# Kernel optimization log

Measured on AMD Instinct MI355X. Metric: run time of the kernel, lower is better.

## Reference

```python
import jax, jax.numpy as jnp
import numpy as np
import math

D_MODEL = 512
NHEAD = 8
D_HEAD = D_MODEL // NHEAD
D_FF = 2048
N_LAYERS = 6
B, S = 8, 2048
EPS = 1e-5


def _layernorm(x, g, b):
    mu = jnp.mean(x, axis=-1, keepdims=True)
    var = jnp.mean(jnp.square(x - mu), axis=-1, keepdims=True)
    return (x - mu) * jax.lax.rsqrt(var + EPS) * g + b


def setup_inputs() -> dict:
    key = jax.random.key(0)
    ks = jax.random.split(key, 10)
    sc = 1.0 / math.sqrt(D_MODEL)
    scf = 1.0 / math.sqrt(D_FF)
    return {
        "x": jax.random.normal(ks[0], (B, S, D_MODEL), jnp.float32),
        "wq": jax.random.normal(ks[1], (N_LAYERS, D_MODEL, D_MODEL), jnp.float32) * sc,
        "wk": jax.random.normal(ks[2], (N_LAYERS, D_MODEL, D_MODEL), jnp.float32) * sc,
        "wv": jax.random.normal(ks[3], (N_LAYERS, D_MODEL, D_MODEL), jnp.float32) * sc,
        "wo": jax.random.normal(ks[4], (N_LAYERS, D_MODEL, D_MODEL), jnp.float32) * sc,
        "w1": jax.random.normal(ks[5], (N_LAYERS, D_MODEL, D_FF), jnp.float32) * sc,
        "b1": jnp.zeros((N_LAYERS, D_FF), jnp.float32),
        "w2": jax.random.normal(ks[6], (N_LAYERS, D_FF, D_MODEL), jnp.float32) * scf,
        "b2": jnp.zeros((N_LAYERS, D_MODEL), jnp.float32),
        "g1": jnp.ones((N_LAYERS, D_MODEL), jnp.float32),
        "beta1": jnp.zeros((N_LAYERS, D_MODEL), jnp.float32),
        "g2": jnp.ones((N_LAYERS, D_MODEL), jnp.float32),
        "beta2": jnp.zeros((N_LAYERS, D_MODEL), jnp.float32),
    }


def reference(x, wq, wk, wv, wo, w1, b1, w2, b2, g1, beta1, g2, beta2):
    scale = 1.0 / math.sqrt(D_HEAD)
    for i in range(N_LAYERS):
        # NOTE: faithful to torch .view(B, nhead, -1, d_head) WITHOUT transpose
        q = (x @ wq[i]).reshape(B, NHEAD, S, D_HEAD)
        k = (x @ wk[i]).reshape(B, NHEAD, S, D_HEAD)
        v = (x @ wv[i]).reshape(B, NHEAD, S, D_HEAD)
        u = jnp.einsum("bhsd,bhtd->bhst", q, k) * scale
        attn = jax.nn.softmax(u, axis=-1)
        o = jnp.einsum("bhst,bhtd->bhsd", attn, v).reshape(B, S, D_MODEL)
        x = _layernorm(x + o @ wo[i], g1[i], beta1[i])
        f = jax.nn.relu(x @ w1[i] + b1[i]) @ w2[i] + b2[i]
        x = _layernorm(x + f, g2[i], beta2[i])
    return x
```

## Files before the change

### kernel.cpp

```cpp
#include <hip/hip_runtime.h>
#include <hip/hip_bf16.h>
#include <stdint.h>

typedef __bf16 bf16_t;
typedef bf16_t bf16x8 __attribute__((ext_vector_type(8)));
typedef bf16_t bf16x4 __attribute__((ext_vector_type(4)));
typedef float  f32x4  __attribute__((ext_vector_type(4)));

#define AS1 __attribute__((address_space(1)))
#define AS3 __attribute__((address_space(3)))

__device__ __forceinline__ void gload_lds16(const void* g, void* l) {
  __builtin_amdgcn_global_load_lds((const AS1 void*)g, (AS3 void*)l, 16, 0, 0);
}

__device__ __forceinline__ float fast_exp2(float x) {
#if __has_builtin(__builtin_amdgcn_exp2f)
  return __builtin_amdgcn_exp2f(x);
#else
  return exp2f(x);
#endif
}

#define QSCALE 0.1803368801111204f

template <int RELU, int BIAS, int QKV>
__global__ __launch_bounds__(256) void gemm_bt(const bf16_t* __restrict__ A,
                                               const bf16_t* __restrict__ Bt,
                                               const float* __restrict__ bias,
                                               bf16_t* __restrict__ Cv,
                                               int M, int N, int K, int ldc) {
  __shared__ __align__(16) char smem[65536];
  const int t = threadIdx.x;
  const int l = t & 63;
  const int w = t >> 6;
  const int wm = w >> 1, wn = w & 1;
  const int lr = l & 15, lg = l >> 4;
  const long m0 = (long)blockIdx.y * 128;
  const long n0 = (long)blockIdx.x * 128;

  const bf16_t* asrc[4];
  const bf16_t* bsrc[4];
#pragma unroll
  for (int it = 0; it < 4; ++it) {
    int y = it * 4096 + t * 16;
    int row = y >> 7;
    int col = ((y & 127) ^ ((row & 7) << 4)) >> 1;
    asrc[it] = A + (m0 + row) * (long)K + col;
    bsrc[it] = Bt + (n0 + row) * (long)K + col;
  }

  auto stage = [&](int buf) {
    char* sb = smem + buf * 32768;
#pragma unroll
    for (int it = 0; it < 4; ++it) {
      gload_lds16(asrc[it], sb + it * 4096 + t * 16);
      gload_lds16(bsrc[it], sb + 16384 + it * 4096 + t * 16);
      asrc[it] += 64;
      bsrc[it] += 64;
    }
  };

  f32x4 acc[4][4] = {};

  stage(0);
  __syncthreads();
  const int nt = K >> 6;
  int buf = 0;
  for (int kt = 0; kt < nt; ++kt) {
    if (kt + 1 < nt) stage(buf ^ 1);
    char* sb = smem + buf * 32768;
#pragma unroll
    for (int kk = 0; kk < 2; ++kk) {
      const int c2 = (kk * 32 + lg * 8) * 2;
      bf16x8 a[4], b[4];
#pragma unroll
      for (int i = 0; i < 4; ++i) {
        int ra = wm * 64 + i * 16 + lr;
        a[i] = *(const bf16x8*)(sb + ((ra * 128 + c2) ^ ((ra & 7) << 4)));
        int rb = wn * 64 + i * 16 + lr;
        b[i] = *(const bf16x8*)(sb + 16384 + ((rb * 128 + c2) ^ ((rb & 7) << 4)));
      }
      __builtin_amdgcn_s_setprio(1);
#pragma unroll
      for (int i = 0; i < 4; ++i)
#pragma unroll
        for (int j = 0; j < 4; ++j)
          acc[i][j] = __builtin_amdgcn_mfma_f32_16x16x32_bf16(a[i], b[j], acc[i][j], 0, 0, 0);
      __builtin_amdgcn_s_setprio(0);
    }
    __syncthreads();
    buf ^= 1;
  }

  float bv[4];
  if (BIAS) {
#pragma unroll
    for (int j = 0; j < 4; ++j) bv[j] = bias[n0 + wn * 64 + j * 16 + lr];
  }
#pragma unroll
  for (int i = 0; i < 4; ++i) {
    long rowb = m0 + wm * 64 + i * 16 + lg * 4;
#pragma unroll
    for (int j = 0; j < 4; ++j) {
      int colbase = (int)n0 + wn * 64 + j * 16;
      bf16_t* outp;
      int coll;
      if (QKV) {
        outp = Cv + (size_t)(colbase >> 9) * 8388608;
        coll = (colbase & 511) + lr;
      } else {
        outp = Cv;
        coll = colbase + lr;
      }
#pragma unroll
      for (int r = 0; r < 4; ++r) {
        float v = acc[i][j][r];
        if (BIAS) v += bv[j];
        if (RELU) v = v > 0.f ? v : 0.f;
        outp[(rowb + r) * (long)ldc + coll] = (bf16_t)v;
      }
    }
  }
}

__global__ __launch_bounds__(256) void attn_fa(const bf16_t* __restrict__ qg,
                                               const bf16_t* __restrict__ kg,
                                               const bf16_t* __restrict__ vg,
                                               bf16_t* __restrict__ og) {
  __shared__ __align__(16) char smem[32768];
  const int t = threadIdx.x, l = t & 63, w = t >> 6;
  const int lr = l & 15, lg = l >> 4;
  const long hoff = (long)blockIdx.x * 131072;
  const int q0 = blockIdx.y * 128 + w * 32;
  const uint32_t LDSB = (uint32_t)(uintptr_t)(AS3 char*)smem;

  bf16x8 qf[2][2];
#pragma unroll
  for (int nf = 0; nf < 2; ++nf)
#pragma unroll
    for (int kk = 0; kk < 2; ++kk)
      qf[nf][kk] = *(const bf16x8*)(qg + hoff + (long)(q0 + nf * 16 + lr) * 64 + kk * 32 + lg * 8);

  const bf16_t* ksrc[2];
#pragma unroll
  for (int i = 0; i < 2; ++i) {
    int y = i * 4096 + t * 16;
    int row = y >> 7;
    int col = ((y & 127) ^ ((row & 7) << 4)) >> 1;
    ksrc[i] = kg + hoff + (long)row * 64 + col;
  }
  const bf16_t* vsrc[2];
#pragma unroll
  for (int i = 0; i < 2; ++i) {
    int y = i * 4096 + t * 16;
    int kk = y >> 12;
    int nj = (y >> 10) & 3;
    int jhi = (y >> 9) & 1;
    int lgs = (y >> 7) & 3;
    int r = (y >> 5) & 3;
    int ch = (y >> 4) & 1;
    int kv = kk * 32 + jhi * 16 + lgs * 4 + r;
    int d0 = nj * 16 + ch * 8;
    vsrc[i] = vg + hoff + (long)kv * 64 + d0;
  }

  auto stage = [&](int buf) {
    char* sb = smem + buf * 16384;
    gload_lds16(ksrc[0], sb + t * 16);
    gload_lds16(ksrc[1], sb + 4096 + t * 16);
    gload_lds16(vsrc[0], sb + 8192 + t * 16);
    gload_lds16(vsrc[1], sb + 12288 + t * 16);
    ksrc[0] += 4096; ksrc[1] += 4096; vsrc[0] += 4096; vsrc[1] += 4096;
  };

  f32x4 oacc[2][4] = {};
  f32x4 lacc[2] = {};
  bf16x8 onesf;
#pragma unroll
  for (int j = 0; j < 8; ++j) onesf[j] = (bf16_t)1.0f;

  stage(0);
  __syncthreads();
  int buf = 0;
  for (int ti = 0; ti < 32; ++ti) {
    if (ti < 31) stage(buf ^ 1);
    char* sb = smem + buf * 16384;

    f32x4 sT[4][2] = {};
#pragma unroll
    for (int kk = 0; kk < 2; ++kk) {
      const int c2 = (kk * 32 + lg * 8) * 2;
      bf16x8 kf[4];
#pragma unroll
      for (int mf = 0; mf < 4; ++mf) {
        int rk = mf * 16 + lr;
        kf[mf] = *(const bf16x8*)(sb + ((rk * 128 + c2) ^ ((rk & 7) << 4)));
      }
      __builtin_amdgcn_s_setprio(1);
#pragma unroll
      for (int mf = 0; mf < 4; ++mf)
#pragma unroll
        for (int nf = 0; nf < 2; ++nf)
          sT[mf][nf] = __builtin_amdgcn_mfma_f32_16x16x32_bf16(kf[mf], qf[nf][kk], sT[mf][nf], 0, 0, 0);
      __builtin_amdgcn_s_setprio(0);
    }

    bf16x8 pa[2][2];
#pragma unroll
    for (int m2 = 0; m2 < 2; ++m2)
#pragma unroll
      for (int kk = 0; kk < 2; ++kk)
#pragma unroll
        for (int jh = 0; jh < 2; ++jh)
#pragma unroll
          for (int r = 0; r < 4; ++r)
            pa[m2][kk][jh * 4 + r] = (bf16_t)fast_exp2(sT[2 * kk + jh][m2][r]);

#pragma unroll
    for (int kk = 0; kk < 2; ++kk) {
      uint32_t va = LDSB + (uint32_t)buf * 16384u + 8192u + (uint32_t)kk * 4096u + (uint32_t)l * 8u;
      bf16x4 v00, v01, v10, v11, v20, v21, v30, v31;
      asm volatile(
          "ds_read_b64_tr_b16 %0, %8 offset:0\n\t"
          "ds_read_b64_tr_b16 %1, %8 offset:512\n\t"
          "ds_read_b64_tr_b16 %2, %8 offset:1024\n\t"
          "ds_read_b64_tr_b16 %3, %8 offset:1536\n\t"
          "ds_read_b64_tr_b16 %4, %8 offset:2048\n\t"
          "ds_read_b64_tr_b16 %5, %8 offset:2560\n\t"
          "ds_read_b64_tr_b16 %6, %8 offset:3072\n\t"
          "ds_read_b64_tr_b16 %7, %8 offset:3584\n\t"
          "s_waitcnt lgkmcnt(0)"
          : "=&v"(v00), "=&v"(v01), "=&v"(v10), "=&v"(v11),
            "=&v"(v20), "=&v"(v21), "=&v"(v30), "=&v"(v31)
          : "v"(va));
      __builtin_amdgcn_sched_barrier(0);
      bf16x8 vf[4];
      vf[0] = __builtin_shufflevector(v00, v01, 0, 1, 2, 3, 4, 5, 6, 7);
      vf[1] = __builtin_shufflevector(v10, v11, 0, 1, 2, 3, 4, 5, 6, 7);
      vf[2] = __builtin_shufflevector(v20, v21, 0, 1, 2, 3, 4, 5, 6, 7);
      vf[3] = __builtin_shufflevector(v30, v31, 0, 1, 2, 3, 4, 5, 6, 7);
      __builtin_amdgcn_s_setprio(1);
#pragma unroll
      for (int m2 = 0; m2 < 2; ++m2) {
#pragma unroll
        for (int nj = 0; nj < 4; ++nj)
          oacc[m2][nj] = __builtin_amdgcn_mfma_f32_16x16x32_bf16(pa[m2][kk], vf[nj], oacc[m2][nj], 0, 0, 0);
        lacc[m2] = __builtin_amdgcn_mfma_f32_16x16x32_bf16(pa[m2][kk], onesf, lacc[m2], 0, 0, 0);
      }
      __builtin_amdgcn_s_setprio(0);
    }
    __syncthreads();
    buf ^= 1;
  }

#pragma unroll
  for (int m2 = 0; m2 < 2; ++m2)
#pragma unroll
    for (int r = 0; r < 4; ++r) {
      float inv = 1.f / lacc[m2][r];
      long row = q0 + m2 * 16 + lg * 4 + r;
#pragma unroll
      for (int nj = 0; nj < 4; ++nj)
        og[hoff + row * 64 + nj * 16 + lr] = (bf16_t)(oacc[m2][nj][r] * inv);
    }
}

__global__ __launch_bounds__(256) void transpose_w(const float* __restrict__ src,
                                                   bf16_t* __restrict__ dst,
                                                   int K, int N,
                                                   long dstLayerStride, float scale) {
  __shared__ float tile[32][33];
  const int t = threadIdx.x;
  const int tx = t & 31, ty = t >> 5;
  const long ls = (long)blockIdx.z * K * N;
  const long ld = (long)blockIdx.z * dstLayerStride;
  const int n0 = blockIdx.x * 32, k0 = blockIdx.y * 32;
#pragma unroll
  for (int i = 0; i < 4; ++i)
    tile[ty + i * 8][tx] = src[ls + (long)(k0 + ty + i * 8) * N + n0 + tx];
  __syncthreads();
#pragma unroll
  for (int i = 0; i < 4; ++i)
    dst[ld + (long)(n0 + ty + i * 8) * K + k0 + tx] = (bf16_t)(tile[tx][ty + i * 8] * scale);
}

__global__ __launch_bounds__(256) void init_x(const float* __restrict__ x,
                                              float* __restrict__ xm,
                                              bf16_t* __restrict__ xb) {
  long i = ((long)blockIdx.x * 256 + threadIdx.x) * 8;
  f32x4 a = *(const f32x4*)(x + i);
  f32x4 b = *(const f32x4*)(x + i + 4);
  *(f32x4*)(xm + i) = a;
  *(f32x4*)(xm + i + 4) = b;
  bf16x8 o;
#pragma unroll
  for (int j = 0; j < 4; ++j) { o[j] = (bf16_t)a[j]; o[4 + j] = (bf16_t)b[j]; }
  *(bf16x8*)(xb + i) = o;
}

__global__ __launch_bounds__(256) void resid_ln(const bf16_t* __restrict__ delta,
                                                float* __restrict__ xm,
                                                bf16_t* __restrict__ xb,
                                                const float* __restrict__ g,
                                                const float* __restrict__ b) {
  const int t = threadIdx.x, l = t & 63, w = t >> 6;
  const long row = (long)blockIdx.x * 4 + w;
  const long base = row * 512 + l * 8;
  f32x4 a0 = *(const f32x4*)(xm + base);
  f32x4 a1 = *(const f32x4*)(xm + base + 4);
  bf16x8 dv = *(const bf16x8*)(delta + base);
  float s[8];
  float sum = 0.f, sq = 0.f;
#pragma unroll
  for (int j = 0; j < 4; ++j) {
    s[j] = a0[j] + (float)dv[j];
    s[4 + j] = a1[j] + (float)dv[4 + j];
  }
#pragma unroll
  for (int j = 0; j < 8; ++j) { sum += s[j]; sq += s[j] * s[j]; }
#pragma unroll
  for (int m = 1; m <= 32; m <<= 1) {
    sum += __shfl_xor(sum, m, 64);
    sq += __shfl_xor(sq, m, 64);
  }
  float mu = sum * (1.f / 512.f);
  float var = sq * (1.f / 512.f) - mu * mu;
  float rstd = rsqrtf(var + 1e-5f);
  f32x4 g0 = *(const f32x4*)(g + l * 8);
  f32x4 g1v = *(const f32x4*)(g + l * 8 + 4);
  f32x4 b0 = *(const f32x4*)(b + l * 8);
  f32x4 b1v = *(const f32x4*)(b + l * 8 + 4);
  f32x4 y0, y1;
  bf16x8 yb;
#pragma unroll
  for (int j = 0; j < 4; ++j) {
    y0[j] = (s[j] - mu) * rstd * g0[j] + b0[j];
    y1[j] = (s[4 + j] - mu) * rstd * g1v[j] + b1v[j];
    yb[j] = (bf16_t)y0[j];
    yb[4 + j] = (bf16_t)y1[j];
  }
  *(f32x4*)(xm + base) = y0;
  *(f32x4*)(xm + base + 4) = y1;
  *(bf16x8*)(xb + base) = yb;
}

extern "C" void kernel_launch(void* const* d_in, const int* in_sizes, int n_in,
                              void* d_out, int out_size, void* d_ws, size_t ws_size,
                              hipStream_t stream) {
  const float* x = (const float*)d_in[0];
  const float* wq = (const float*)d_in[1];
  const float* wk = (const float*)d_in[2];
  const float* wv = (const float*)d_in[3];
  const float* wo = (const float*)d_in[4];
  const float* w1 = (const float*)d_in[5];
  const float* b1 = (const float*)d_in[6];
  const float* w2 = (const float*)d_in[7];
  const float* b2 = (const float*)d_in[8];
  const float* g1 = (const float*)d_in[9];
  const float* be1 = (const float*)d_in[10];
  const float* g2 = (const float*)d_in[11];
  const float* be2 = (const float*)d_in[12];

  float* xm = (float*)d_out;
  char* ws = (char*)d_ws;

  const int M = 16384, D = 512, DFF = 2048, NL = 6;
  const size_t sz_small = (size_t)NL * D * D * 2;
  const size_t sz_big = (size_t)NL * D * DFF * 2;
  bf16_t* wqkvt = (bf16_t*)(ws);
  bf16_t* wot = (bf16_t*)(ws + 3 * sz_small);
  bf16_t* w1t = (bf16_t*)(ws + 4 * sz_small);
  bf16_t* w2t = (bf16_t*)(ws + 4 * sz_small + sz_big);
  char* actbase = ws + 4 * sz_small + 2 * sz_big;
  bf16_t* xb = (bf16_t*)(actbase);
  char* R = actbase + (size_t)M * D * 2;
  bf16_t* qb = (bf16_t*)(R);
  bf16_t* kb = (bf16_t*)(R + (size_t)M * D * 2);
  bf16_t* vb = (bf16_t*)(R + 2 * (size_t)M * D * 2);
  bf16_t* ob = (bf16_t*)(R + 3 * (size_t)M * D * 2);
  bf16_t* hb = (bf16_t*)(R);
  bf16_t* tmpb = (bf16_t*)(R + 4 * (size_t)M * D * 2);

  const long LQKV = 1536L * 512;
  transpose_w<<<dim3(D / 32, D / 32, NL), 256, 0, stream>>>(wq, wqkvt, D, D, LQKV, QSCALE);
  transpose_w<<<dim3(D / 32, D / 32, NL), 256, 0, stream>>>(wk, wqkvt + 512 * 512, D, D, LQKV, 1.f);
  transpose_w<<<dim3(D / 32, D / 32, NL), 256, 0, stream>>>(wv, wqkvt + 2 * 512 * 512, D, D, LQKV, 1.f);
  transpose_w<<<dim3(D / 32, D / 32, NL), 256, 0, stream>>>(wo, wot, D, D, (long)D * D, 1.f);
  transpose_w<<<dim3(DFF / 32, D / 32, NL), 256, 0, stream>>>(w1, w1t, D, DFF, (long)D * DFF, 1.f);
  transpose_w<<<dim3(D / 32, DFF / 32, NL), 256, 0, stream>>>(w2, w2t, DFF, D, (long)D * DFF, 1.f);
  init_x<<<4096, 256, 0, stream>>>(x, xm, xb);

  for (int L = 0; L < NL; ++L) {
    const bf16_t* wqkvL = wqkvt + (size_t)L * LQKV;
    const bf16_t* woL = wot + (size_t)L * D * D;
    const bf16_t* w1L = w1t + (size_t)L * D * DFF;
    const bf16_t* w2L = w2t + (size_t)L * D * DFF;

    gemm_bt<0, 0, 1><<<dim3(12, 128), 256, 0, stream>>>(xb, wqkvL, nullptr, qb, M, 1536, D, 512);
    attn_fa<<<dim3(64, 16), 256, 0, stream>>>(qb, kb, vb, ob);
    gemm_bt<0, 0, 0><<<dim3(4, 128), 256, 0, stream>>>(ob, woL, nullptr, tmpb, M, D, D, D);
    resid_ln<<<4096, 256, 0, stream>>>(tmpb, xm, xb, g1 + L * D, be1 + L * D);
    gemm_bt<1, 1, 0><<<dim3(16, 128), 256, 0, stream>>>(xb, w1L, b1 + (size_t)L * DFF, hb, M, DFF, D, DFF);
    gemm_bt<0, 1, 0><<<dim3(4, 128), 256, 0, stream>>>(hb, w2L, b2 + L * D, tmpb, M, D, DFF, D);
    resid_ln<<<4096, 256, 0, stream>>>(tmpb, xm, xb, g2 + L * D, be2 + L * D);
  }
}
```

Measured before the change: 1.649 ms.

## Swizzle block order, add single-buffer GEMM variant, batch V transposed reads

```diff
diff --git a/kernel.cpp b/kernel.cpp
--- a/kernel.cpp
+++ b/kernel.cpp
@@ -24,20 +24,25 @@
 
 #define QSCALE 0.1803368801111204f
 
-template <int RELU, int BIAS, int QKV>
+template <int RELU, int BIAS, int QKV, int DBUF>
 __global__ __launch_bounds__(256) void gemm_bt(const bf16_t* __restrict__ A,
                                                const bf16_t* __restrict__ Bt,
                                                const float* __restrict__ bias,
                                                bf16_t* __restrict__ Cv,
                                                int M, int N, int K, int ldc) {
-  __shared__ __align__(16) char smem[65536];
+  __shared__ __align__(16) char smem[DBUF ? 65536 : 32768];
   const int t = threadIdx.x;
   const int l = t & 63;
   const int w = t >> 6;
   const int wm = w >> 1, wn = w & 1;
   const int lr = l & 15, lg = l >> 4;
-  const long m0 = (long)blockIdx.y * 128;
-  const long n0 = (long)blockIdx.x * 128;
+
+  const int gx = gridDim.x;
+  const int nwg = gx * gridDim.y;
+  const int orig = blockIdx.y * gx + blockIdx.x;
+  const int swz = (orig & 7) * (nwg >> 3) + (orig >> 3);
+  const long m0 = (long)(swz / gx) * 128;
+  const long n0 = (long)(swz % gx) * 128;
 
   const bf16_t* asrc[4];
   const bf16_t* bsrc[4];
@@ -62,14 +67,9 @@
   };
 
   f32x4 acc[4][4] = {};
-
-  stage(0);
-  __syncthreads();
   const int nt = K >> 6;
-  int buf = 0;
-  for (int kt = 0; kt < nt; ++kt) {
-    if (kt + 1 < nt) stage(buf ^ 1);
-    char* sb = smem + buf * 32768;
+
+  auto compute = [&](char* sb) {
 #pragma unroll
     for (int kk = 0; kk < 2; ++kk) {
       const int c2 = (kk * 32 + lg * 8) * 2;
@@ -89,8 +89,25 @@
           acc[i][j] = __builtin_amdgcn_mfma_f32_16x16x32_bf16(a[i], b[j], acc[i][j], 0, 0, 0);
       __builtin_amdgcn_s_setprio(0);
     }
+  };
+
+  if (DBUF) {
+    stage(0);
     __syncthreads();
-    buf ^= 1;
+    int buf = 0;
+    for (int kt = 0; kt < nt; ++kt) {
+      if (kt + 1 < nt) stage(buf ^ 1);
+      compute(smem + buf * 32768);
+      __syncthreads();
+      buf ^= 1;
+    }
+  } else {
+    for (int kt = 0; kt < nt; ++kt) {
+      __syncthreads();
+      stage(0);
+      __syncthreads();
+      compute(smem);
+    }
   }
 
   float bv[4];
@@ -131,8 +148,10 @@
   __shared__ __align__(16) char smem[32768];
   const int t = threadIdx.x, l = t & 63, w = t >> 6;
   const int lr = l & 15, lg = l >> 4;
-  const long hoff = (long)blockIdx.x * 131072;
-  const int q0 = blockIdx.y * 128 + w * 32;
+  const int lin = blockIdx.x;
+  const int swz = (lin & 7) * 128 + (lin >> 3);
+  const long hoff = (long)(swz >> 4) * 131072;
+  const int q0 = (swz & 15) * 128 + w * 32;
   const uint32_t LDSB = (uint32_t)(uintptr_t)(AS3 char*)smem;
 
   bf16x8 qf[2][2];
@@ -206,50 +225,73 @@
       __builtin_amdgcn_s_setprio(0);
     }
 
+    uint32_t va = LDSB + (uint32_t)buf * 16384u + 8192u + (uint32_t)l * 8u;
+    bf16x4 tv0, tv1, tv2, tv3, tv4, tv5, tv6, tv7;
+    bf16x4 tv8, tv9, tva, tvb, tvc, tvd, tve, tvf;
+    asm volatile(
+        "ds_read_b64_tr_b16 %0, %16 offset:0\n\t"
+        "ds_read_b64_tr_b16 %1, %16 offset:512\n\t"
+        "ds_read_b64_tr_b16 %2, %16 offset:1024\n\t"
+        "ds_read_b64_tr_b16 %3, %16 offset:1536\n\t"
+        "ds_read_b64_tr_b16 %4, %16 offset:2048\n\t"
+        "ds_read_b64_tr_b16 %5, %16 offset:2560\n\t"
+        "ds_read_b64_tr_b16 %6, %16 offset:3072\n\t"
+        "ds_read_b64_tr_b16 %7, %16 offset:3584\n\t"
+        "ds_read_b64_tr_b16 %8, %16 offset:4096\n\t"
+        "ds_read_b64_tr_b16 %9, %16 offset:4608\n\t"
+        "ds_read_b64_tr_b16 %10, %16 offset:5120\n\t"
+        "ds_read_b64_tr_b16 %11, %16 offset:5632\n\t"
+        "ds_read_b64_tr_b16 %12, %16 offset:6144\n\t"
+        "ds_read_b64_tr_b16 %13, %16 offset:6656\n\t"
+        "ds_read_b64_tr_b16 %14, %16 offset:7168\n\t"
+        "ds_read_b64_tr_b16 %15, %16 offset:7680"
+        : "=&v"(tv0), "=&v"(tv1), "=&v"(tv2), "=&v"(tv3),
+          "=&v"(tv4), "=&v"(tv5), "=&v"(tv6), "=&v"(tv7),
+          "=&v"(tv8), "=&v"(tv9), "=&v"(tva), "=&v"(tvb),
+          "=&v"(tvc), "=&v"(tvd), "=&v"(tve), "=&v"(tvf)
+        : "v"(va));
+
     bf16x8 pa[2][2];
 #pragma unroll
     for (int m2 = 0; m2 < 2; ++m2)
 #pragma unroll
-      for (int kk = 0; kk < 2; ++kk)
-#pragma unroll
-        for (int jh = 0; jh < 2; ++jh)
-#pragma unroll
-          for (int r = 0; r < 4; ++r)
-            pa[m2][kk][jh * 4 + r] = (bf16_t)fast_exp2(sT[2 * kk + jh][m2][r]);
-
-#pragma unroll
-    for (int kk = 0; kk < 2; ++kk) {
-      uint32_t va = LDSB + (uint32_t)buf * 16384u + 8192u + (uint32_t)kk * 4096u + (uint32_t)l * 8u;
-      bf16x4 v00, v01, v10, v11, v20, v21, v30, v31;
-      asm volatile(
-          "ds_read_b64_tr_b16 %0, %8 offset:0\n\t"
-          "ds_read_b64_tr_b16 %1, %8 offset:512\n\t"
-          "ds_read_b64_tr_b16 %2, %8 offset:1024\n\t"
-          "ds_read_b64_tr_b16 %3, %8 offset:1536\n\t"
-          "ds_read_b64_tr_b16 %4, %8 offset:2048\n\t"
-          "ds_read_b64_tr_b16 %5, %8 offset:2560\n\t"
-          "ds_read_b64_tr_b16 %6, %8 offset:3072\n\t"
-          "ds_read_b64_tr_b16 %7, %8 offset:3584\n\t"
-          "s_waitcnt lgkmcnt(0)"
-          : "=&v"(v00), "=&v"(v01), "=&v"(v10), "=&v"(v11),
-            "=&v"(v20), "=&v"(v21), "=&v"(v30), "=&v"(v31)
-          : "v"(va));
-      __builtin_amdgcn_sched_barrier(0);
-      bf16x8 vf[4];
-      vf[0] = __builtin_shufflevector(v00, v01, 0, 1, 2, 3, 4, 5, 6, 7);
-      vf[1] = __builtin_shufflevector(v10, v11, 0, 1, 2, 3, 4, 5, 6, 7);
-      vf[2] = __builtin_shufflevector(v20, v21, 0, 1, 2, 3, 4, 5, 6, 7);
-      vf[3] = __builtin_shufflevector(v30, v31, 0, 1, 2, 3, 4, 5, 6, 7);
-      __builtin_amdgcn_s_setprio(1);
+      for (int kk = 0; kk < 2; ++kk) {
+        f32x4 e0, e1;
+#pragma unroll
+        for (int r = 0; r < 4; ++r) {
+          e0[r] = fast_exp2(sT[2 * kk][m2][r]);
+          e1[r] = fast_exp2(sT[2 * kk + 1][m2][r]);
+        }
+        bf16x4 c0 = __builtin_convertvector(e0, bf16x4);
+        bf16x4 c1 = __builtin_convertvector(e1, bf16x4);
+        pa[m2][kk] = __builtin_shufflevector(c0, c1, 0, 1, 2, 3, 4, 5, 6, 7);
+      }
+
+    asm volatile("s_waitcnt lgkmcnt(0)" ::: "memory");
+    __builtin_amdgcn_sched_barrier(0);
+
+    bf16x8 vf[2][4];
+    vf[0][0] = __builtin_shufflevector(tv0, tv1, 0, 1, 2, 3, 4, 5, 6, 7);
+    vf[0][1] = __builtin_shufflevector(tv2, tv3, 0, 1, 2, 3, 4, 5, 6, 7);
+    vf[0][2] = __builtin_shufflevector(tv4, tv5, 0, 1, 2, 3, 4, 5, 6, 7);
+    vf[0][3] = __builtin_shufflevector(tv6, tv7, 0, 1, 2, 3, 4, 5, 6, 7);
+    vf[1][0] = __builtin_shufflevector(tv8, tv9, 0, 1, 2, 3, 4, 5, 6, 7);
+    vf[1][1] = __builtin_shufflevector(tva, tvb, 0, 1, 2, 3, 4, 5, 6, 7);
+    vf[1][2] = __builtin_shufflevector(tvc, tvd, 0, 1, 2, 3, 4, 5, 6, 7);
+    vf[1][3] = __builtin_shufflevector(tve, tvf, 0, 1, 2, 3, 4, 5, 6, 7);
+
+    __builtin_amdgcn_s_setprio(1);
+#pragma unroll
+    for (int kk = 0; kk < 2; ++kk)
 #pragma unroll
       for (int m2 = 0; m2 < 2; ++m2) {
 #pragma unroll
         for (int nj = 0; nj < 4; ++nj)
-          oacc[m2][nj] = __builtin_amdgcn_mfma_f32_16x16x32_bf16(pa[m2][kk], vf[nj], oacc[m2][nj], 0, 0, 0);
+          oacc[m2][nj] = __builtin_amdgcn_mfma_f32_16x16x32_bf16(pa[m2][kk], vf[kk][nj], oacc[m2][nj], 0, 0, 0);
         lacc[m2] = __builtin_amdgcn_mfma_f32_16x16x32_bf16(pa[m2][kk], onesf, lacc[m2], 0, 0, 0);
       }
-      __builtin_amdgcn_s_setprio(0);
-    }
+    __builtin_amdgcn_s_setprio(0);
+
     __syncthreads();
     buf ^= 1;
   }
@@ -397,12 +439,12 @@
     const bf16_t* w1L = w1t + (size_t)L * D * DFF;
     const bf16_t* w2L = w2t + (size_t)L * D * DFF;
 
-    gemm_bt<0, 0, 1><<<dim3(12, 128), 256, 0, stream>>>(xb, wqkvL, nullptr, qb, M, 1536, D, 512);
-    attn_fa<<<dim3(64, 16), 256, 0, stream>>>(qb, kb, vb, ob);
-    gemm_bt<0, 0, 0><<<dim3(4, 128), 256, 0, stream>>>(ob, woL, nullptr, tmpb, M, D, D, D);
+    gemm_bt<0, 0, 1, 0><<<dim3(12, 128), 256, 0, stream>>>(xb, wqkvL, nullptr, qb, M, 1536, D, 512);
+    attn_fa<<<dim3(1024), 256, 0, stream>>>(qb, kb, vb, ob);
+    gemm_bt<0, 0, 0, 1><<<dim3(4, 128), 256, 0, stream>>>(ob, woL, nullptr, tmpb, M, D, D, D);
     resid_ln<<<4096, 256, 0, stream>>>(tmpb, xm, xb, g1 + L * D, be1 + L * D);
-    gemm_bt<1, 1, 0><<<dim3(16, 128), 256, 0, stream>>>(xb, w1L, b1 + (size_t)L * DFF, hb, M, DFF, D, DFF);
-    gemm_bt<0, 1, 0><<<dim3(4, 128), 256, 0, stream>>>(hb, w2L, b2 + L * D, tmpb, M, D, DFF, D);
+    gemm_bt<1, 1, 0, 0><<<dim3(16, 128), 256, 0, stream>>>(xb, w1L, b1 + (size_t)L * DFF, hb, M, DFF, D, DFF);
+    gemm_bt<0, 1, 0, 1><<<dim3(4, 128), 256, 0, stream>>>(hb, w2L, b2 + L * D, tmpb, M, D, DFF, D);
     resid_ln<<<4096, 256, 0, stream>>>(tmpb, xm, xb, g2 + L * D, be2 + L * D);
   }
 }
```

Result: faster. 1.571 ms (-4.7%).
